# Optimization experiments

Measured on AMD Instinct MI355X. Metric: run time of the kernel, lower is better.

The kernel has to match this reference:

```python
import jax, jax.numpy as jnp
from jax import lax
import numpy as np

B, Q, T, C = 64, 900, 100, 92
W_CLASS, W_BBOX, W_GIOU = 1.0, 1.0, 1.0


def to_corners(b):
    cx, cy, w, h = b[..., 0], b[..., 1], b[..., 2], b[..., 3]
    return jnp.stack([cx - 0.5 * w, cy - 0.5 * h, cx + 0.5 * w, cy + 0.5 * h], axis=-1)


def generalized_iou(b1, b2):
    # b1 [Q,4], b2 [T,4] in corner format -> pairwise GIoU [Q,T]
    a1 = (b1[:, 2] - b1[:, 0]) * (b1[:, 3] - b1[:, 1])
    a2 = (b2[:, 2] - b2[:, 0]) * (b2[:, 3] - b2[:, 1])
    lt = jnp.maximum(b1[:, None, :2], b2[None, :, :2])
    rb = jnp.minimum(b1[:, None, 2:], b2[None, :, 2:])
    wh = jnp.clip(rb - lt, 0.0)
    inter = wh[..., 0] * wh[..., 1]
    union = a1[:, None] + a2[None, :] - inter
    iou = inter / union
    lt_e = jnp.minimum(b1[:, None, :2], b2[None, :, :2])
    rb_e = jnp.maximum(b1[:, None, 2:], b2[None, :, 2:])
    wh_e = jnp.clip(rb_e - lt_e, 0.0)
    area_e = wh_e[..., 0] * wh_e[..., 1]
    return iou - (area_e - union) / area_e


def cost_matrix(logits, pred_bbox, tgt_labels, tgt_bbox):
    conf = jax.nn.softmax(logits, axis=-1)                                  # [B,Q,C]
    cost_class = -jax.vmap(lambda c, l: c[:, l])(conf, tgt_labels)          # [B,Q,T]
    cost_bbox = jnp.sum(jnp.abs(pred_bbox[:, :, None, :] - tgt_bbox[:, None, :, :]), axis=-1)
    cost_giou = -jax.vmap(generalized_iou)(to_corners(pred_bbox), to_corners(tgt_bbox))
    return W_BBOX * cost_bbox + W_CLASS * cost_class + W_GIOU * cost_giou   # [B,Q,T]


def solve_lsa(cost):
    # Jonker-Volgenant shortest-augmenting-path optimal assignment.
    # cost [n, m] with n <= m; assigns every row to a distinct column.
    n, m = cost.shape
    INF = jnp.asarray(1e9, cost.dtype)

    def assign_row(i, carry):
        u, v, p = carry        # u [n+1], v [m+1] potentials; p [m+1]: row assigned to col (0=free)
        p = p.at[0].set(i + 1)
        minv0 = jnp.full(m + 1, INF, cost.dtype)
        used0 = jnp.zeros(m + 1, bool)
        way0 = jnp.zeros(m + 1, jnp.int32)

        def cond(s):
            j0, u, v, p, minv, used, way = s
            return p[j0] != 0

        def body(s):
            j0, u, v, p, minv, used, way = s
            used = used.at[j0].set(True)
            i0 = p[j0]
            cur = cost[i0 - 1] - u[i0] - v[1:]          # reduced costs over cols 1..m
            cur = jnp.where(used[1:], INF, cur)
            better = cur < minv[1:]
            minv = minv.at[1:].set(jnp.where(better, cur, minv[1:]))
            way = way.at[1:].set(jnp.where(better, j0, way[1:]))
            masked = jnp.where(used[1:], INF, minv[1:])
            j1 = jnp.argmin(masked).astype(jnp.int32) + 1
            delta = masked[j1 - 1]
            u = u.at[p].add(jnp.where(used, delta, jnp.zeros((), cost.dtype)))
            v = v - jnp.where(used, delta, jnp.zeros((), cost.dtype))
            minv = minv - jnp.where(used, jnp.zeros((), cost.dtype), delta)
            return j1, u, v, p, minv, used, way

        j0, u, v, p, _, _, way = lax.while_loop(
            cond, body, (jnp.int32(0), u, v, p, minv0, used0, way0))

        def aug_cond(s):
            jj, p = s
            return jj != 0

        def aug_body(s):
            jj, p = s
            j1 = way[jj]
            p = p.at[jj].set(p[j1])
            return j1, p

        _, p = lax.while_loop(aug_cond, aug_body, (j0, p))
        return u, v, p

    u0 = jnp.zeros(n + 1, cost.dtype)
    v0 = jnp.zeros(m + 1, cost.dtype)
    p0 = jnp.zeros(m + 1, jnp.int32)
    _, _, p = lax.fori_loop(0, n, assign_row, (u0, v0, p0))
    # column (0-based) assigned to each row i
    q = jnp.argmax(p[1:, None] == (jnp.arange(n, dtype=jnp.int32) + 1)[None, :], axis=0)
    order = jnp.argsort(q)
    return q[order].astype(jnp.int32), order.astype(jnp.int32)


def setup_inputs() -> dict:
    key = jax.random.key(0)
    k1, k2, k3, k4 = jax.random.split(key, 4)
    return {
        'logits': jax.random.normal(k1, (B, Q, C), jnp.float32),
        'pred_bbox': jax.random.uniform(k2, (B, Q, 4), jnp.float32),
        'tgt_labels': jax.random.randint(k3, (B, T), 0, C, jnp.int32),
        'tgt_bbox': jax.random.uniform(k4, (B, T, 4), jnp.float32),
    }


def reference(logits, pred_bbox, tgt_labels, tgt_bbox):
    cost = cost_matrix(logits, pred_bbox, tgt_labels, tgt_bbox)   # [B,Q,T]
    # scipy solves the [Q,T] problem (Q > T): transpose so rows (targets) <= cols (queries).
    row_ind, col_ind = jax.vmap(lambda c: solve_lsa(c.T))(cost)
    # row_ind: query indices (ascending), col_ind: matched target indices, per image.
    return cost, row_ind, col_ind
```

## Files before the change

kernel.cpp:

```cpp
#include <hip/hip_runtime.h>
#include <cmath>

#define Bq 64
#define Qn 900
#define Tn 100
#define Cn 92
#define INFN 1e9f
#define QT 64
#define NQT 15
#define NTJ 256

__global__ __launch_bounds__(256) void cost_fused_kernel(
        const float* __restrict__ logits,
        const float* __restrict__ pred_bbox,
        const int*   __restrict__ tgt_labels,
        const float* __restrict__ tgt_bbox,
        float* __restrict__ cost,
        float* __restrict__ costT)
{
    const int b   = blockIdx.y;
    const int q0  = blockIdx.x * QT;
    const int nq  = (q0 + QT <= Qn) ? QT : (Qn - q0);
    const int tid = threadIdx.x;

    __shared__ float prob[QT * Cn];
    __shared__ float pb_s[QT][4];
    __shared__ float tb_s[Tn][4];
    __shared__ int   lab_s[Tn];
    __shared__ float ctile[QT][Tn + 1];

    const float* lg_src = logits + ((size_t)b * Qn + q0) * Cn;
    for (int idx = tid; idx < nq * Cn; idx += 256) prob[idx] = lg_src[idx];
    for (int idx = tid; idx < nq * 4; idx += 256)
        ((float*)pb_s)[idx] = pred_bbox[((size_t)b * Qn + q0) * 4 + idx];
    for (int idx = tid; idx < Tn * 4; idx += 256)
        ((float*)tb_s)[idx] = tgt_bbox[(size_t)b * Tn * 4 + idx];
    for (int idx = tid; idx < Tn; idx += 256)
        lab_s[idx] = tgt_labels[b * Tn + idx];
    __syncthreads();

    const int g = tid >> 2, l4 = tid & 3;
    if (g < nq) {
        float mx = -3.0e38f;
        for (int c = l4; c < Cn; c += 4) mx = fmaxf(mx, prob[g * Cn + c]);
        mx = fmaxf(mx, __shfl_xor(mx, 1));
        mx = fmaxf(mx, __shfl_xor(mx, 2));
        float s = 0.0f;
        for (int c = l4; c < Cn; c += 4) s += expf(prob[g * Cn + c] - mx);
        s += __shfl_xor(s, 1);
        s += __shfl_xor(s, 2);
        float inv = 1.0f / s;
        for (int c = l4; c < Cn; c += 4)
            prob[g * Cn + c] = expf(prob[g * Cn + c] - mx) * inv;
    }
    __syncthreads();

    const int total = nq * Tn;
    float* cdst = cost + (size_t)b * Qn * Tn + (size_t)q0 * Tn;
    for (int flat = tid; flat < total; flat += 256) {
        int q = flat / Tn, tt = flat - q * Tn;
        float pcx = pb_s[q][0], pcy = pb_s[q][1], pw = pb_s[q][2], ph = pb_s[q][3];
        float tcx = tb_s[tt][0], tcy = tb_s[tt][1], tw = tb_s[tt][2], th = tb_s[tt][3];

        float cclass = -prob[q * Cn + lab_s[tt]];
        float cbbox  = fabsf(pcx - tcx) + fabsf(pcy - tcy)
                     + fabsf(pw - tw)  + fabsf(ph - th);

        float px1 = pcx - 0.5f * pw, py1 = pcy - 0.5f * ph;
        float px2 = pcx + 0.5f * pw, py2 = pcy + 0.5f * ph;
        float tx1 = tcx - 0.5f * tw, ty1 = tcy - 0.5f * th;
        float tx2 = tcx + 0.5f * tw, ty2 = tcy + 0.5f * th;

        float a1 = (px2 - px1) * (py2 - py1);
        float a2 = (tx2 - tx1) * (ty2 - ty1);
        float iw = fmaxf(fminf(px2, tx2) - fmaxf(px1, tx1), 0.0f);
        float ih = fmaxf(fminf(py2, ty2) - fmaxf(py1, ty1), 0.0f);
        float inter = iw * ih;
        float uni = a1 + a2 - inter;
        float iou = inter / uni;
        float ew = fmaxf(fmaxf(px2, tx2) - fminf(px1, tx1), 0.0f);
        float eh = fmaxf(fmaxf(py2, ty2) - fminf(py1, ty1), 0.0f);
        float ae = ew * eh;
        float val = cbbox + cclass - (iou - (ae - uni) / ae);

        cdst[flat] = val;
        ctile[q][tt] = val;
    }
    if (costT) {
        __syncthreads();
        float* tdst = costT + (size_t)b * Qn * Tn + q0;
        if (nq == QT) {
            for (int flat = tid; flat < QT * Tn; flat += 256) {
                int r = flat >> 6, c = flat & 63;
                tdst[(size_t)r * Qn + c] = ctile[c][r];
            }
        } else {
            for (int flat = tid; flat < nq * Tn; flat += 256) {
                int r = flat / nq, c = flat - r * nq;
                tdst[(size_t)r * Qn + c] = ctile[c][r];
            }
        }
    }
}

template<bool TRANS>
__global__ __launch_bounds__(NTJ) void jv_kernel(
        const float* __restrict__ cost,
        float* __restrict__ out)
{
    const int b    = blockIdx.x;
    const int tid  = threadIdx.x;
    const int lane = tid & 63;
    const int wv   = tid >> 6;
    const bool act = (tid < Qn / 4);

    __shared__ int   p_lds[Qn + 1];
    __shared__ int   way_lds[Qn + 1];
    __shared__ float u_lds[Tn + 1];
    __shared__ int   amin_lds[Tn];
    __shared__ unsigned char asg[Tn];
    __shared__ int   freelist[Tn];
    __shared__ int   nfree_s;
    __shared__ float redv[2][4];
    __shared__ int   redj[2][4];
    __shared__ int   qarr[Tn];

    for (int j = tid; j <= Qn; j += NTJ) p_lds[j] = 0;
    if (tid == 0) nfree_s = 0;
    __syncthreads();

    const float* cb = cost + (size_t)b * Qn * Tn;

    for (int r = wv; r < Tn; r += 4) {
        float bv = 3.0e38f; int bj = 0x3fffffff;
        #pragma unroll
        for (int k = 0; k < 15; ++k) {
            int c = lane + 64 * k;
            if (c < Qn) {
                float x = TRANS ? cb[(size_t)r * Qn + c] : cb[(size_t)c * Tn + r];
                if (x < bv) { bv = x; bj = c; }
            }
        }
        #pragma unroll
        for (int off = 1; off < 64; off <<= 1) {
            float ov = __shfl_xor(bv, off);
            int   oj = __shfl_xor(bj, off);
            if (ov < bv || (ov == bv && oj < bj)) { bv = ov; bj = oj; }
        }
        if (lane == 0) { u_lds[r + 1] = bv; amin_lds[r] = bj; }
    }
    __syncthreads();

    if (tid < Tn) {
        int j = amin_lds[tid];
        int old = atomicCAS(&p_lds[j + 1], 0, tid + 1);
        asg[tid] = (old == 0) ? 1 : 0;
    }
    __syncthreads();
    if (tid < Tn && !asg[tid]) {
        int s = atomicAdd(&nfree_s, 1);
        freelist[s] = tid;
    }
    __syncthreads();
    const int nfree = nfree_s;

    const int cbase = 4 * tid;
    float varr[4] = {0.0f, 0.0f, 0.0f, 0.0f};

    for (int s = 0; s < nfree; ++s) {
        const int ri = freelist[s];
        float minv[4] = {INFN, INFN, INFN, INFN};
        unsigned um = 0;
        int i0 = ri + 1, j0 = 0;
        if (tid == 0) p_lds[0] = i0;

        float c0v = 0, c1v = 0, c2v = 0, c3v = 0;
        if (act) {
            if (TRANS) {
                float4 cr = *(const float4*)(cb + (size_t)(i0 - 1) * Qn + cbase);
                c0v = cr.x; c1v = cr.y; c2v = cr.z; c3v = cr.w;
            } else {
                const float* cp = cb + (i0 - 1);
                c0v = cp[(size_t)cbase * Tn];       c1v = cp[(size_t)(cbase + 1) * Tn];
                c2v = cp[(size_t)(cbase + 2) * Tn]; c3v = cp[(size_t)(cbase + 3) * Tn];
            }
        }
        float ui0 = u_lds[i0];

        for (int it = 0; it < Tn + 2; ++it) {
            if (j0 > 0 && act) {
                int cc = j0 - 1;
                if ((cc >> 2) == tid) um |= 1u << (cc & 3);
            }
            float bv = 3.0e9f; int bj = 0x3fffffff;
            if (act) {
                float crr[4] = {c0v, c1v, c2v, c3v};
                #pragma unroll
                for (int k = 0; k < 4; ++k) {
                    if (!((um >> k) & 1u)) {
                        float cur = crr[k] - ui0 - varr[k];
                        if (cur < minv[k]) { minv[k] = cur; way_lds[cbase + k + 1] = j0; }
                        if (minv[k] < bv) { bv = minv[k]; bj = cbase + k + 1; }
                    }
                }
            }
            #pragma unroll
            for (int off = 1; off < 64; off <<= 1) {
                float ov = __shfl_xor(bv, off);
                int   oj = __shfl_xor(bj, off);
                if (ov < bv || (ov == bv && oj < bj)) { bv = ov; bj = oj; }
            }
            const int par = it & 1;
            if (lane == 0) { redv[par][wv] = bv; redj[par][wv] = bj; }
            __syncthreads();
            float delta = redv[par][0]; int bestj = redj[par][0];
            #pragma unroll
            for (int w = 1; w < 4; ++w) {
                float ov = redv[par][w]; int oj = redj[par][w];
                if (ov < delta || (ov == delta && oj < bestj)) { delta = ov; bestj = oj; }
            }
            const int bp = p_lds[bestj];

            float ui_n = 0.0f, n0 = 0, n1 = 0, n2 = 0, n3 = 0;
            if (bp != 0) {
                if (act) {
                    if (TRANS) {
                        float4 cr = *(const float4*)(cb + (size_t)(bp - 1) * Qn + cbase);
                        n0 = cr.x; n1 = cr.y; n2 = cr.z; n3 = cr.w;
                    } else {
                        const float* cp = cb + (bp - 1);
                        n0 = cp[(size_t)cbase * Tn];       n1 = cp[(size_t)(cbase + 1) * Tn];
                        n2 = cp[(size_t)(cbase + 2) * Tn]; n3 = cp[(size_t)(cbase + 3) * Tn];
                    }
                }
                ui_n = u_lds[bp];
            }

            if (tid == 0) u_lds[ri + 1] += delta;
            if (act) {
                #pragma unroll
                for (int k = 0; k < 4; ++k) {
                    if ((um >> k) & 1u) {
                        varr[k] -= delta;
                        u_lds[p_lds[cbase + k + 1]] += delta;
                    } else {
                        minv[k] -= delta;
                    }
                }
            }
            j0 = bestj;
            if (bp == 0) break;
            i0 = bp; ui0 = ui_n;
            c0v = n0; c1v = n1; c2v = n2; c3v = n3;
        }

        if (tid == 0) {
            int jj = j0;
            while (jj != 0) { int j1 = way_lds[jj]; p_lds[jj] = p_lds[j1]; jj = j1; }
        }
        __syncthreads();
    }

    for (int j = tid + 1; j <= Qn; j += NTJ) {
        int r = p_lds[j];
        if (r) qarr[r - 1] = j - 1;
    }
    __syncthreads();

    float* out_row = out + (size_t)Bq * Qn * Tn + (size_t)b * Tn;
    float* out_col = out_row + (size_t)Bq * Tn;
    for (int i = tid; i < Tn; i += NTJ) {
        int qi = qarr[i];
        int rank = 0;
        for (int jj = 0; jj < Tn; ++jj) rank += (qarr[jj] < qi) ? 1 : 0;
        out_row[rank] = (float)qi;
        out_col[rank] = (float)i;
    }
}

extern "C" void kernel_launch(void* const* d_in, const int* in_sizes, int n_in,
                              void* d_out, int out_size, void* d_ws, size_t ws_size,
                              hipStream_t stream) {
    const float* logits     = (const float*)d_in[0];
    const float* pred_bbox  = (const float*)d_in[1];
    const int*   tgt_labels = (const int*)d_in[2];
    const float* tgt_bbox   = (const float*)d_in[3];
    float* out = (float*)d_out;

    const size_t needT = (size_t)Bq * Qn * Tn * sizeof(float);
    float* costT = (ws_size >= needT) ? (float*)d_ws : nullptr;

    hipLaunchKernelGGL(cost_fused_kernel, dim3(NQT, Bq), dim3(256), 0, stream,
                       logits, pred_bbox, tgt_labels, tgt_bbox, out, costT);
    if (costT) {
        hipLaunchKernelGGL((jv_kernel<true>), dim3(Bq), dim3(NTJ), 0, stream,
                           costT, out);
    } else {
        hipLaunchKernelGGL((jv_kernel<false>), dim3(Bq), dim3(NTJ), 0, stream,
                           out, out);
    }
}
```

Baseline: 106.2 us.

## Run JV augmentation in a single wavefront with DPP min and fused tile minima

The shortest-augmenting-path loop now runs in one 64-lane wavefront, with each lane holding 16 columns in registers. This removes the per-iteration __syncthreads and cross-wave LDS reduction. The argmin uses an order-preserving float key, a DPP wave-min and a ballot instead of a shuffle butterfly. The cost kernel also writes per-tile column minima, so the JV init can skip rescanning the transposed cost, and the softmax no longer recomputes exp. The price is a serial single-wave dependency chain with heavier per-lane register work, plus extra workspace and a global store.

```diff
diff --git a/kernel.cpp b/kernel.cpp
--- a/kernel.cpp
+++ b/kernel.cpp
@@ -8,7 +8,31 @@
 #define INFN 1e9f
 #define QT 64
 #define NQT 15
-#define NTJ 256
+
+__device__ inline unsigned fkey(float x) {
+    unsigned u = __float_as_uint(x);
+    return (u & 0x80000000u) ? ~u : (u | 0x80000000u);
+}
+__device__ inline float unfkey(unsigned k) {
+    unsigned u = (k & 0x80000000u) ? (k & 0x7FFFFFFFu) : ~k;
+    return __uint_as_float(u);
+}
+
+__device__ inline unsigned wave_min_u32(unsigned x) {
+    unsigned t;
+#define DPPSTEP(ctrl)                                                          \
+    t = (unsigned)__builtin_amdgcn_update_dpp((int)0xFFFFFFFF, (int)x, ctrl,   \
+                                              0xF, 0xF, false);                \
+    x = (t < x) ? t : x;
+    DPPSTEP(0x111)
+    DPPSTEP(0x112)
+    DPPSTEP(0x114)
+    DPPSTEP(0x118)
+    DPPSTEP(0x142)
+    DPPSTEP(0x143)
+#undef DPPSTEP
+    return (unsigned)__builtin_amdgcn_readlane((int)x, 63);
+}
 
 __global__ __launch_bounds__(256) void cost_fused_kernel(
         const float* __restrict__ logits,
@@ -16,7 +40,8 @@
         const int*   __restrict__ tgt_labels,
         const float* __restrict__ tgt_bbox,
         float* __restrict__ cost,
-        float* __restrict__ costT)
+        float* __restrict__ costT,
+        unsigned long long* __restrict__ tilemin)
 {
     const int b   = blockIdx.y;
     const int q0  = blockIdx.x * QT;
@@ -46,12 +71,15 @@
         mx = fmaxf(mx, __shfl_xor(mx, 1));
         mx = fmaxf(mx, __shfl_xor(mx, 2));
         float s = 0.0f;
-        for (int c = l4; c < Cn; c += 4) s += expf(prob[g * Cn + c] - mx);
+        for (int c = l4; c < Cn; c += 4) {
+            float e = expf(prob[g * Cn + c] - mx);
+            prob[g * Cn + c] = e;
+            s += e;
+        }
         s += __shfl_xor(s, 1);
         s += __shfl_xor(s, 2);
         float inv = 1.0f / s;
-        for (int c = l4; c < Cn; c += 4)
-            prob[g * Cn + c] = expf(prob[g * Cn + c] - mx) * inv;
+        for (int c = l4; c < Cn; c += 4) prob[g * Cn + c] *= inv;
     }
     __syncthreads();
 
@@ -86,8 +114,9 @@
         cdst[flat] = val;
         ctile[q][tt] = val;
     }
+    __syncthreads();
+
     if (costT) {
-        __syncthreads();
         float* tdst = costT + (size_t)b * Qn * Tn + q0;
         if (nq == QT) {
             for (int flat = tid; flat < QT * Tn; flat += 256) {
@@ -101,10 +130,203 @@
             }
         }
     }
-}
-
-template<bool TRANS>
-__global__ __launch_bounds__(NTJ) void jv_kernel(
+    if (tilemin && tid < Tn) {
+        float bvv = 3.0e38f; int bq = 0;
+        for (int q = 0; q < nq; ++q) {
+            float x = ctile[q][tid];
+            if (x < bvv) { bvv = x; bq = q; }
+        }
+        tilemin[((size_t)b * NQT + blockIdx.x) * Tn + tid] =
+            ((unsigned long long)fkey(bvv) << 32) | (unsigned)(q0 + bq);
+    }
+}
+
+template<bool TM>
+__global__ __launch_bounds__(256) void jv_kernel(
+        const float* __restrict__ costT,
+        const unsigned long long* __restrict__ tilemin,
+        float* __restrict__ out)
+{
+    const int b    = blockIdx.x;
+    const int tid  = threadIdx.x;
+    const int lane = tid & 63;
+    const int wv   = tid >> 6;
+
+    __shared__ int   p_lds[Qn + 1];
+    __shared__ int   way_lds[1024];
+    __shared__ float u_lds[Tn + 1];
+    __shared__ int   amin_lds[Tn];
+    __shared__ unsigned char asg[Tn];
+    __shared__ int   freelist[Tn];
+    __shared__ int   nfree_s;
+    __shared__ int   qarr[Tn];
+
+    for (int j = tid; j <= Qn; j += 256) p_lds[j] = 0;
+    if (tid == 0) nfree_s = 0;
+    __syncthreads();
+
+    const float* cb = costT + (size_t)b * Qn * Tn;
+
+    if (TM) {
+        if (tid < Tn) {
+            unsigned long long best = ~0ull;
+            for (int t = 0; t < NQT; ++t) {
+                unsigned long long v = tilemin[((size_t)b * NQT + t) * Tn + tid];
+                if (v < best) best = v;
+            }
+            u_lds[tid + 1] = unfkey((unsigned)(best >> 32));
+            amin_lds[tid]  = (int)(best & 0xFFFFFFFFu);
+        }
+    } else {
+        for (int r = wv; r < Tn; r += 4) {
+            float bv = 3.0e38f; int bj = 0x3fffffff;
+            #pragma unroll
+            for (int k = 0; k < 15; ++k) {
+                int c = lane + 64 * k;
+                if (c < Qn) {
+                    float x = cb[(size_t)r * Qn + c];
+                    if (x < bv) { bv = x; bj = c; }
+                }
+            }
+            #pragma unroll
+            for (int off = 1; off < 64; off <<= 1) {
+                float ov = __shfl_xor(bv, off);
+                int   oj = __shfl_xor(bj, off);
+                if (ov < bv || (ov == bv && oj < bj)) { bv = ov; bj = oj; }
+            }
+            if (lane == 0) { u_lds[r + 1] = bv; amin_lds[r] = bj; }
+        }
+    }
+    __syncthreads();
+
+    if (tid < Tn) {
+        int j = amin_lds[tid];
+        int old = atomicCAS(&p_lds[j + 1], 0, tid + 1);
+        asg[tid] = (old == 0) ? 1 : 0;
+    }
+    __syncthreads();
+    if (tid < Tn && !asg[tid]) {
+        int s = atomicAdd(&nfree_s, 1);
+        freelist[s] = tid;
+    }
+    __syncthreads();
+    const int nfree = nfree_s;
+
+    if (wv == 0 && nfree > 0) {
+        const int cbase = lane << 4;
+        float v_r[16], minv_r[16], rc[16], rn[16];
+        #pragma unroll
+        for (int k = 0; k < 16; ++k) v_r[k] = 0.0f;
+
+#define LOADROW(dst, row1)                                                     \
+        {                                                                      \
+            const float* rp = cb + (size_t)((row1) - 1) * Qn;                  \
+            if (cbase + 16 <= Qn) {                                            \
+                _Pragma("unroll")                                              \
+                for (int w4 = 0; w4 < 4; ++w4) {                               \
+                    float4 f = *(const float4*)(rp + cbase + 4 * w4);          \
+                    dst[4*w4+0] = f.x; dst[4*w4+1] = f.y;                      \
+                    dst[4*w4+2] = f.z; dst[4*w4+3] = f.w;                      \
+                }                                                              \
+            } else {                                                           \
+                _Pragma("unroll")                                              \
+                for (int k = 0; k < 16; ++k)                                   \
+                    dst[k] = (cbase + k < Qn) ? rp[cbase + k] : 3.0e38f;       \
+            }                                                                  \
+        }
+
+        for (int s = 0; s < nfree; ++s) {
+            const int ri = freelist[s];
+            unsigned um = 0;
+            #pragma unroll
+            for (int k = 0; k < 16; ++k) minv_r[k] = 3.0e38f;
+            int i0 = ri + 1, j0 = 0;
+            if (lane == 0) p_lds[0] = i0;
+            LOADROW(rc, i0);
+            float ui0 = u_lds[i0];
+
+            for (int it = 0; it < Tn + 2; ++it) {
+                if (j0 > 0) {
+                    int cc = j0 - 1;
+                    if ((cc >> 4) == lane) um |= 1u << (cc & 15);
+                }
+                float bv = 3.0e38f; int bj = 0;
+                #pragma unroll
+                for (int k = 0; k < 16; ++k) {
+                    int c = cbase + k;
+                    if (c < Qn && !((um >> k) & 1u)) {
+                        float cur = rc[k] - ui0 - v_r[k];
+                        if (cur < minv_r[k]) {
+                            minv_r[k] = cur;
+                            way_lds[(k << 6) | lane] = j0;
+                        }
+                        if (minv_r[k] < bv) { bv = minv_r[k]; bj = c; }
+                    }
+                }
+                unsigned tk = fkey(bv);
+                unsigned gk = wave_min_u32(tk);
+                unsigned long long msk = __ballot(tk == gk);
+                int src = __ffsll(msk) - 1;
+                int bestj = __shfl(bj, src) + 1;
+                float delta = __shfl(bv, src);
+                int bp = p_lds[bestj];
+
+                float un = 0.0f;
+                if (bp != 0) { LOADROW(rn, bp); un = u_lds[bp]; }
+
+                if (lane == 0) u_lds[ri + 1] += delta;
+                #pragma unroll
+                for (int k = 0; k < 16; ++k) {
+                    int c = cbase + k;
+                    if (c < Qn) {
+                        if ((um >> k) & 1u) {
+                            v_r[k] -= delta;
+                            u_lds[p_lds[c + 1]] += delta;
+                        } else {
+                            minv_r[k] -= delta;
+                        }
+                    }
+                }
+                j0 = bestj;
+                if (bp == 0) break;
+                i0 = bp; ui0 = un;
+                #pragma unroll
+                for (int k = 0; k < 16; ++k) rc[k] = rn[k];
+            }
+
+            if (lane == 0) {
+                int jj = j0;
+                while (jj != 0) {
+                    int cc = jj - 1;
+                    int j1 = way_lds[((cc & 15) << 6) | (cc >> 4)];
+                    p_lds[jj] = p_lds[j1];
+                    jj = j1;
+                }
+            }
+            __threadfence_block();
+        }
+#undef LOADROW
+    }
+    __syncthreads();
+
+    for (int j = tid + 1; j <= Qn; j += 256) {
+        int r = p_lds[j];
+        if (r) qarr[r - 1] = j - 1;
+    }
+    __syncthreads();
+
+    float* out_row = out + (size_t)Bq * Qn * Tn + (size_t)b * Tn;
+    float* out_col = out_row + (size_t)Bq * Tn;
+    for (int i = tid; i < Tn; i += 256) {
+        int qi = qarr[i];
+        int rank = 0;
+        for (int jj = 0; jj < Tn; ++jj) rank += (qarr[jj] < qi) ? 1 : 0;
+        out_row[rank] = (float)qi;
+        out_col[rank] = (float)i;
+    }
+}
+
+__global__ __launch_bounds__(256) void jv_compat_kernel(
         const float* __restrict__ cost,
         float* __restrict__ out)
 {
@@ -125,7 +347,7 @@
     __shared__ int   redj[2][4];
     __shared__ int   qarr[Tn];
 
-    for (int j = tid; j <= Qn; j += NTJ) p_lds[j] = 0;
+    for (int j = tid; j <= Qn; j += 256) p_lds[j] = 0;
     if (tid == 0) nfree_s = 0;
     __syncthreads();
 
@@ -137,7 +359,7 @@
         for (int k = 0; k < 15; ++k) {
             int c = lane + 64 * k;
             if (c < Qn) {
-                float x = TRANS ? cb[(size_t)r * Qn + c] : cb[(size_t)c * Tn + r];
+                float x = cb[(size_t)c * Tn + r];
                 if (x < bv) { bv = x; bj = c; }
             }
         }
@@ -176,14 +398,9 @@
 
         float c0v = 0, c1v = 0, c2v = 0, c3v = 0;
         if (act) {
-            if (TRANS) {
-                float4 cr = *(const float4*)(cb + (size_t)(i0 - 1) * Qn + cbase);
-                c0v = cr.x; c1v = cr.y; c2v = cr.z; c3v = cr.w;
-            } else {
-                const float* cp = cb + (i0 - 1);
-                c0v = cp[(size_t)cbase * Tn];       c1v = cp[(size_t)(cbase + 1) * Tn];
-                c2v = cp[(size_t)(cbase + 2) * Tn]; c3v = cp[(size_t)(cbase + 3) * Tn];
-            }
+            const float* cp = cb + (i0 - 1);
+            c0v = cp[(size_t)cbase * Tn];       c1v = cp[(size_t)(cbase + 1) * Tn];
+            c2v = cp[(size_t)(cbase + 2) * Tn]; c3v = cp[(size_t)(cbase + 3) * Tn];
         }
         float ui0 = u_lds[i0];
 
@@ -224,14 +441,9 @@
             float ui_n = 0.0f, n0 = 0, n1 = 0, n2 = 0, n3 = 0;
             if (bp != 0) {
                 if (act) {
-                    if (TRANS) {
-                        float4 cr = *(const float4*)(cb + (size_t)(bp - 1) * Qn + cbase);
-                        n0 = cr.x; n1 = cr.y; n2 = cr.z; n3 = cr.w;
-                    } else {
-                        const float* cp = cb + (bp - 1);
-                        n0 = cp[(size_t)cbase * Tn];       n1 = cp[(size_t)(cbase + 1) * Tn];
-                        n2 = cp[(size_t)(cbase + 2) * Tn]; n3 = cp[(size_t)(cbase + 3) * Tn];
-                    }
+                    const float* cp = cb + (bp - 1);
+                    n0 = cp[(size_t)cbase * Tn];       n1 = cp[(size_t)(cbase + 1) * Tn];
+                    n2 = cp[(size_t)(cbase + 2) * Tn]; n3 = cp[(size_t)(cbase + 3) * Tn];
                 }
                 ui_n = u_lds[bp];
             }
@@ -261,7 +473,7 @@
         __syncthreads();
     }
 
-    for (int j = tid + 1; j <= Qn; j += NTJ) {
+    for (int j = tid + 1; j <= Qn; j += 256) {
         int r = p_lds[j];
         if (r) qarr[r - 1] = j - 1;
     }
@@ -269,7 +481,7 @@
 
     float* out_row = out + (size_t)Bq * Qn * Tn + (size_t)b * Tn;
     float* out_col = out_row + (size_t)Bq * Tn;
-    for (int i = tid; i < Tn; i += NTJ) {
+    for (int i = tid; i < Tn; i += 256) {
         int qi = qarr[i];
         int rank = 0;
         for (int jj = 0; jj < Tn; ++jj) rank += (qarr[jj] < qi) ? 1 : 0;
@@ -287,16 +499,28 @@
     const float* tgt_bbox   = (const float*)d_in[3];
     float* out = (float*)d_out;
 
-    const size_t needT = (size_t)Bq * Qn * Tn * sizeof(float);
-    float* costT = (ws_size >= needT) ? (float*)d_ws : nullptr;
-
-    hipLaunchKernelGGL(cost_fused_kernel, dim3(NQT, Bq), dim3(256), 0, stream,
-                       logits, pred_bbox, tgt_labels, tgt_bbox, out, costT);
-    if (costT) {
-        hipLaunchKernelGGL((jv_kernel<true>), dim3(Bq), dim3(NTJ), 0, stream,
-                           costT, out);
+    const size_t needT  = (size_t)Bq * Qn * Tn * sizeof(float);
+    const size_t needTM = needT + (size_t)Bq * NQT * Tn * 8 + 4096;
+
+    if (ws_size >= needTM) {
+        float* costT = (float*)d_ws;
+        unsigned long long* tilemin = (unsigned long long*)((char*)d_ws + needT);
+        hipLaunchKernelGGL(cost_fused_kernel, dim3(NQT, Bq), dim3(256), 0, stream,
+                           logits, pred_bbox, tgt_labels, tgt_bbox, out, costT, tilemin);
+        hipLaunchKernelGGL((jv_kernel<true>), dim3(Bq), dim3(256), 0, stream,
+                           costT, tilemin, out);
+    } else if (ws_size >= needT) {
+        float* costT = (float*)d_ws;
+        hipLaunchKernelGGL(cost_fused_kernel, dim3(NQT, Bq), dim3(256), 0, stream,
+                           logits, pred_bbox, tgt_labels, tgt_bbox, out, costT,
+                           (unsigned long long*)nullptr);
+        hipLaunchKernelGGL((jv_kernel<false>), dim3(Bq), dim3(256), 0, stream,
+                           costT, (const unsigned long long*)nullptr, out);
     } else {
-        hipLaunchKernelGGL((jv_kernel<false>), dim3(Bq), dim3(NTJ), 0, stream,
+        hipLaunchKernelGGL(cost_fused_kernel, dim3(NQT, Bq), dim3(256), 0, stream,
+                           logits, pred_bbox, tgt_labels, tgt_bbox, out,
+                           (float*)nullptr, (unsigned long long*)nullptr);
+        hipLaunchKernelGGL(jv_compat_kernel, dim3(Bq), dim3(256), 0, stream,
                            out, out);
     }
 }
```

Result: slower. 111.0 us (+4.5%).
